# Performance work log

Measured on AMD Instinct MI355X. Metric: run time of the kernel, lower is better.

## Reference

```python
import jax, jax.numpy as jnp
import numpy as np

EPS_LN = 1e-6
EPS_COS = 1e-8  # torch F.cosine_similarity default eps


def setup_inputs() -> dict:
    key = jax.random.key(0)
    ks = jax.random.split(key, 6)
    in_dim, hidden, out_dim, b = 1024, 512, 128, 8192
    x = jax.random.normal(ks[0], (b, in_dim), dtype=jnp.float32)
    # Linear layers: torch default init ~ U(-1/sqrt(fan_in), 1/sqrt(fan_in))
    w1 = jax.random.uniform(ks[1], (in_dim, hidden), jnp.float32, -1, 1) / np.sqrt(in_dim)
    b1 = jax.random.uniform(ks[2], (hidden,), jnp.float32, -1, 1) / np.sqrt(in_dim)
    w2 = jax.random.uniform(ks[3], (hidden, out_dim), jnp.float32, -1, 1) / np.sqrt(hidden)
    b2 = jax.random.uniform(ks[4], (out_dim,), jnp.float32, -1, 1) / np.sqrt(hidden)
    prelu_a = jnp.float32(0.25)  # nn.PReLU default: single shared parameter, init 0.25
    ln_gamma = jnp.ones((hidden,), jnp.float32)
    ln_beta = jnp.zeros((hidden,), jnp.float32)
    return {"x": x, "w1": w1, "b1": b1, "prelu_a": prelu_a,
            "ln_gamma": ln_gamma, "ln_beta": ln_beta, "w2": w2, "b2": b2}


def _layer_norm(h, gamma, beta):
    mu = jnp.mean(h, axis=-1, keepdims=True)
    var = jnp.mean(jnp.square(h - mu), axis=-1, keepdims=True)
    return (h - mu) * jax.lax.rsqrt(var + EPS_LN) * gamma + beta


def reference(x, w1, b1, prelu_a, ln_gamma, ln_beta, w2, b2):
    h = x @ w1 + b1                              # [b, hidden]
    h = jnp.where(h >= 0, h, prelu_a * h)        # PReLU
    h = _layer_norm(h, ln_gamma, ln_beta)        # Dropout is identity in reference
    z = h @ w2 + b2                              # [b, out_dim]
    # get_y_hat: full pairwise cosine similarity as normalize + Gram matmul
    norms = jnp.maximum(jnp.linalg.norm(z, axis=1, keepdims=True), EPS_COS)
    zn = z / norms                               # [b, out_dim]
    y_hat = zn @ zn.T                            # [b, b]
    return z, y_hat
```

## Files before the change

kernel.cpp:

```cpp
#include <hip/hip_runtime.h>
#include <stdint.h>

typedef uint16_t u16;
typedef __bf16 bf16x8 __attribute__((ext_vector_type(8)));
typedef float f32x4 __attribute__((ext_vector_type(4)));

__device__ __forceinline__ u16 f2bf(float f) {
  union { float f; uint32_t u; } v; v.f = f;
  uint32_t u = v.u;
  u += 0x7FFFu + ((u >> 16) & 1u);
  return (u16)(u >> 16);
}
__device__ __forceinline__ float bf2f(u16 h) {
  union { uint32_t u; float f; } v; v.u = ((uint32_t)h) << 16; return v.f;
}

__global__ void transpose_both(const float* __restrict__ w1, u16* __restrict__ w1t,
                               const float* __restrict__ w2, u16* __restrict__ w2t) {
  const float* in; u16* out; int R, C;
  if (blockIdx.z == 0) { in = w1; out = w1t; R = 1024; C = 512; }
  else {
    if (blockIdx.x >= 4 || blockIdx.y >= 16) return;
    in = w2; out = w2t; R = 512; C = 128;
  }
  __shared__ float tile[32][33];
  int bx = blockIdx.x * 32, by = blockIdx.y * 32;
  int tx = threadIdx.x, ty = threadIdx.y;
  for (int i = 0; i < 32; i += 8)
    tile[ty + i][tx] = in[(size_t)(by + ty + i) * C + bx + tx];
  __syncthreads();
  for (int i = 0; i < 32; i += 8)
    out[(size_t)(bx + ty + i) * R + by + tx] = f2bf(tile[tx][ty + i]);
}

#define BKT 64

__launch_bounds__(256)
__global__ void gemm1_kernel(const float* __restrict__ A,
                             const u16* __restrict__ Bt,
                             const float* __restrict__ bias,
                             const float* __restrict__ prelu_a,
                             u16* __restrict__ out) {
  const int N = 512, K = 1024;
  __shared__ u16 As[64][BKT + 8];
  __shared__ u16 Bs[128][BKT + 8];
  const int lane = threadIdx.x & 63, wave = threadIdx.x >> 6;
  const int row0 = blockIdx.x * 64, col0 = blockIdx.y * 128;

  f32x4 zero4 = {0.f, 0.f, 0.f, 0.f};
  f32x4 acc[8];
#pragma unroll
  for (int j = 0; j < 8; ++j) acc[j] = zero4;

  for (int k0 = 0; k0 < K; k0 += BKT) {
#pragma unroll
    for (int s = 0; s < 2; ++s) {
      int c = threadIdx.x + s * 256;
      int r = c >> 3, kc = (c & 7) << 3;
      const float4* p = (const float4*)(A + (size_t)(row0 + r) * K + k0 + kc);
      float4 f0 = p[0], f1 = p[1];
      u16 tmp[8] = {f2bf(f0.x), f2bf(f0.y), f2bf(f0.z), f2bf(f0.w),
                    f2bf(f1.x), f2bf(f1.y), f2bf(f1.z), f2bf(f1.w)};
      *(uint4*)(&As[r][kc]) = *(uint4*)tmp;
    }
#pragma unroll
    for (int s = 0; s < 4; ++s) {
      int c = threadIdx.x + s * 256;
      int r = c >> 3, kc = (c & 7) << 3;
      *(uint4*)(&Bs[r][kc]) = *(const uint4*)(Bt + (size_t)(col0 + r) * K + k0 + kc);
    }
    __syncthreads();
#pragma unroll
    for (int kk = 0; kk < BKT; kk += 32) {
      bf16x8 a, b[8];
      a = *(const bf16x8*)(&As[wave * 16 + (lane & 15)][kk + (lane >> 4) * 8]);
#pragma unroll
      for (int j = 0; j < 8; ++j)
        b[j] = *(const bf16x8*)(&Bs[j * 16 + (lane & 15)][kk + (lane >> 4) * 8]);
#pragma unroll
      for (int j = 0; j < 8; ++j)
        acc[j] = __builtin_amdgcn_mfma_f32_16x16x32_bf16(a, b[j], acc[j], 0, 0, 0);
    }
    __syncthreads();
  }

  float ap = *prelu_a;
#pragma unroll
  for (int r = 0; r < 4; ++r) {
    int row = row0 + wave * 16 + (lane >> 4) * 4 + r;
#pragma unroll
    for (int j = 0; j < 8; ++j) {
      int col = col0 + j * 16 + (lane & 15);
      float v = acc[j][r] + bias[col];
      v = v >= 0.f ? v : ap * v;
      out[(size_t)row * N + col] = f2bf(v);
    }
  }
}

__launch_bounds__(256)
__global__ void ln_kernel(const u16* __restrict__ h, const float* __restrict__ gamma,
                          const float* __restrict__ beta, u16* __restrict__ out) {
  int lane = threadIdx.x & 63, wave = threadIdx.x >> 6;
  int row = blockIdx.x * 4 + wave;
  uint4 raw = *(const uint4*)(h + (size_t)row * 512 + lane * 8);
  u16* up = (u16*)&raw;
  float v[8], s = 0.f, s2 = 0.f;
#pragma unroll
  for (int e = 0; e < 8; ++e) { v[e] = bf2f(up[e]); s += v[e]; s2 += v[e] * v[e]; }
  for (int m = 1; m < 64; m <<= 1) { s += __shfl_xor(s, m); s2 += __shfl_xor(s2, m); }
  float mu = s * (1.f / 512.f);
  float var = s2 * (1.f / 512.f) - mu * mu;
  float rstd = rsqrtf(var + 1e-6f);
  u16 o[8];
#pragma unroll
  for (int e = 0; e < 8; ++e) {
    int c = lane * 8 + e;
    o[e] = f2bf((v[e] - mu) * rstd * gamma[c] + beta[c]);
  }
  *(uint4*)(out + (size_t)row * 512 + lane * 8) = *(uint4*)o;
}

__launch_bounds__(256)
__global__ void gemm2_kernel(const u16* __restrict__ A, const u16* __restrict__ Bt,
                             const float* __restrict__ bias,
                             float* __restrict__ z, u16* __restrict__ zn) {
  const int K = 512;
  __shared__ u16 As[32][BKT + 8];
  __shared__ u16 Bs[128][BKT + 8];
  __shared__ float hsum[32][2];
  const int lane = threadIdx.x & 63, wave = threadIdx.x >> 6;
  const int wr = wave >> 1, wc = wave & 1;
  const int row0 = blockIdx.x * 32;

  f32x4 zero4 = {0.f, 0.f, 0.f, 0.f};
  f32x4 acc[4];
#pragma unroll
  for (int j = 0; j < 4; ++j) acc[j] = zero4;

  for (int k0 = 0; k0 < K; k0 += BKT) {
    {
      int r = threadIdx.x >> 3, kc = (threadIdx.x & 7) << 3;
      *(uint4*)(&As[r][kc]) = *(const uint4*)(A + (size_t)(row0 + r) * K + k0 + kc);
    }
#pragma unroll
    for (int s = 0; s < 4; ++s) {
      int c = threadIdx.x + s * 256;
      int r = c >> 3, kc = (c & 7) << 3;
      *(uint4*)(&Bs[r][kc]) = *(const uint4*)(Bt + (size_t)r * K + k0 + kc);
    }
    __syncthreads();
#pragma unroll
    for (int kk = 0; kk < BKT; kk += 32) {
      bf16x8 a, b[4];
      a = *(const bf16x8*)(&As[wr * 16 + (lane & 15)][kk + (lane >> 4) * 8]);
#pragma unroll
      for (int j = 0; j < 4; ++j)
        b[j] = *(const bf16x8*)(&Bs[wc * 64 + j * 16 + (lane & 15)][kk + (lane >> 4) * 8]);
#pragma unroll
      for (int j = 0; j < 4; ++j)
        acc[j] = __builtin_amdgcn_mfma_f32_16x16x32_bf16(a, b[j], acc[j], 0, 0, 0);
    }
    __syncthreads();
  }

  float vv[4][4];
#pragma unroll
  for (int r = 0; r < 4; ++r) {
    float s = 0.f;
#pragma unroll
    for (int j = 0; j < 4; ++j) {
      int col = wc * 64 + j * 16 + (lane & 15);
      float v = acc[j][r] + bias[col];
      vv[r][j] = v; s += v * v;
    }
    s += __shfl_xor(s, 1); s += __shfl_xor(s, 2);
    s += __shfl_xor(s, 4); s += __shfl_xor(s, 8);
    if ((lane & 15) == 0) {
      int rloc = wr * 16 + (lane >> 4) * 4 + r;
      hsum[rloc][wc] = s;
    }
  }
  __syncthreads();
#pragma unroll
  for (int r = 0; r < 4; ++r) {
    int rloc = wr * 16 + (lane >> 4) * 4 + r;
    float s = hsum[rloc][0] + hsum[rloc][1];
    float inv = 1.f / fmaxf(sqrtf(s), 1e-8f);
    int row = row0 + rloc;
#pragma unroll
    for (int j = 0; j < 4; ++j) {
      int col = wc * 64 + j * 16 + (lane & 15);
      z[(size_t)row * 128 + col] = vv[r][j];
      zn[(size_t)row * 128 + col] = f2bf(vv[r][j] * inv);
    }
  }
}

#define GBM 128
#define GBN 128

__launch_bounds__(256)
__global__ void gram_kernel(const u16* __restrict__ Z, float* __restrict__ y) {
  const int K = 128, Bdim = 8192;
  __shared__ u16 As[GBM][BKT + 8];
  __shared__ u16 Bs[GBN][BKT + 8];
  const int lane = threadIdx.x & 63, wave = threadIdx.x >> 6;
  const int row0 = blockIdx.x * GBM, col0 = blockIdx.y * GBN;

  f32x4 zero4 = {0.f, 0.f, 0.f, 0.f};
  f32x4 acc[2][8];
#pragma unroll
  for (int i = 0; i < 2; ++i)
#pragma unroll
    for (int j = 0; j < 8; ++j) acc[i][j] = zero4;

  for (int k0 = 0; k0 < K; k0 += BKT) {
#pragma unroll
    for (int s = 0; s < 4; ++s) {
      int c = threadIdx.x + s * 256;
      int r = c >> 3, kc = (c & 7) << 3;
      *(uint4*)(&As[r][kc]) = *(const uint4*)(Z + (size_t)(row0 + r) * K + k0 + kc);
      *(uint4*)(&Bs[r][kc]) = *(const uint4*)(Z + (size_t)(col0 + r) * K + k0 + kc);
    }
    __syncthreads();
#pragma unroll
    for (int kk = 0; kk < BKT; kk += 32) {
      bf16x8 a[2], b[8];
#pragma unroll
      for (int i = 0; i < 2; ++i)
        a[i] = *(const bf16x8*)(&As[wave * 32 + i * 16 + (lane & 15)][kk + (lane >> 4) * 8]);
#pragma unroll
      for (int j = 0; j < 8; ++j)
        b[j] = *(const bf16x8*)(&Bs[j * 16 + (lane & 15)][kk + (lane >> 4) * 8]);
#pragma unroll
      for (int i = 0; i < 2; ++i)
#pragma unroll
        for (int j = 0; j < 8; ++j)
          acc[i][j] = __builtin_amdgcn_mfma_f32_16x16x32_bf16(a[i], b[j], acc[i][j], 0, 0, 0);
    }
    __syncthreads();
  }

#pragma unroll
  for (int i = 0; i < 2; ++i)
#pragma unroll
    for (int r = 0; r < 4; ++r) {
      int row = row0 + wave * 32 + i * 16 + (lane >> 4) * 4 + r;
#pragma unroll
      for (int j = 0; j < 8; ++j) {
        int col = col0 + j * 16 + (lane & 15);
        y[(size_t)row * Bdim + col] = acc[i][j][r];
      }
    }
}

extern "C" void kernel_launch(void* const* d_in, const int* in_sizes, int n_in,
                              void* d_out, int out_size, void* d_ws, size_t ws_size,
                              hipStream_t stream) {
  const float* x       = (const float*)d_in[0];
  const float* w1      = (const float*)d_in[1];
  const float* b1      = (const float*)d_in[2];
  const float* prelu_a = (const float*)d_in[3];
  const float* gamma   = (const float*)d_in[4];
  const float* beta    = (const float*)d_in[5];
  const float* w2      = (const float*)d_in[6];
  const float* b2      = (const float*)d_in[7];

  float* z_out = (float*)d_out;
  float* yhat  = z_out + (size_t)8192 * 128;

  char* ws = (char*)d_ws;
  u16* w1t  = (u16*)(ws);
  u16* w2t  = (u16*)(ws + (1u << 20));
  u16* hact = (u16*)(ws + (1u << 20) + (1u << 17));
  u16* hln  = (u16*)(ws + (1u << 20) + (1u << 17) + (8u << 20));
  u16* zn   = (u16*)(ws + (1u << 20) + (1u << 17) + (16u << 20));

  transpose_both<<<dim3(16, 32, 2), dim3(32, 8), 0, stream>>>(w1, w1t, w2, w2t);
  gemm1_kernel<<<dim3(128, 4), 256, 0, stream>>>(x, w1t, b1, prelu_a, hact);
  ln_kernel<<<2048, 256, 0, stream>>>(hact, gamma, beta, hln);
  gemm2_kernel<<<256, 256, 0, stream>>>(hln, w2t, b2, z_out, zn);
  gram_kernel<<<dim3(64, 64), 256, 0, stream>>>(zn, yhat);
}
```

Measured before the change: 362.6 us.

## Fold LayerNorm into gemm2 via algebraic mean/rstd correction

```diff
diff --git a/kernel.cpp b/kernel.cpp
--- a/kernel.cpp
+++ b/kernel.cpp
@@ -16,7 +16,23 @@
 }
 
 __global__ void transpose_both(const float* __restrict__ w1, u16* __restrict__ w1t,
-                               const float* __restrict__ w2, u16* __restrict__ w2t) {
+                               const float* __restrict__ w2, u16* __restrict__ w2t,
+                               const float* __restrict__ gamma,
+                               const float* __restrict__ beta,
+                               float* __restrict__ gw2, float* __restrict__ bw2) {
+  if (blockIdx.z == 2) {
+    if (blockIdx.x || blockIdx.y) return;
+    int tid = threadIdx.y * 32 + threadIdx.x;
+    if (tid < 128) {
+      float g = 0.f, b = 0.f;
+      for (int k = 0; k < 512; ++k) {
+        float w = bf2f(f2bf(w2[(size_t)k * 128 + tid]));
+        g += gamma[k] * w; b += beta[k] * w;
+      }
+      gw2[tid] = g; bw2[tid] = b;
+    }
+    return;
+  }
   const float* in; u16* out; int R, C;
   if (blockIdx.z == 0) { in = w1; out = w1t; R = 1024; C = 512; }
   else {
@@ -99,35 +115,17 @@
 }
 
 __launch_bounds__(256)
-__global__ void ln_kernel(const u16* __restrict__ h, const float* __restrict__ gamma,
-                          const float* __restrict__ beta, u16* __restrict__ out) {
-  int lane = threadIdx.x & 63, wave = threadIdx.x >> 6;
-  int row = blockIdx.x * 4 + wave;
-  uint4 raw = *(const uint4*)(h + (size_t)row * 512 + lane * 8);
-  u16* up = (u16*)&raw;
-  float v[8], s = 0.f, s2 = 0.f;
-#pragma unroll
-  for (int e = 0; e < 8; ++e) { v[e] = bf2f(up[e]); s += v[e]; s2 += v[e] * v[e]; }
-  for (int m = 1; m < 64; m <<= 1) { s += __shfl_xor(s, m); s2 += __shfl_xor(s2, m); }
-  float mu = s * (1.f / 512.f);
-  float var = s2 * (1.f / 512.f) - mu * mu;
-  float rstd = rsqrtf(var + 1e-6f);
-  u16 o[8];
-#pragma unroll
-  for (int e = 0; e < 8; ++e) {
-    int c = lane * 8 + e;
-    o[e] = f2bf((v[e] - mu) * rstd * gamma[c] + beta[c]);
-  }
-  *(uint4*)(out + (size_t)row * 512 + lane * 8) = *(uint4*)o;
-}
-
-__launch_bounds__(256)
 __global__ void gemm2_kernel(const u16* __restrict__ A, const u16* __restrict__ Bt,
-                             const float* __restrict__ bias,
+                             const float* __restrict__ b2,
+                             const float* __restrict__ gamma,
+                             const float* __restrict__ gw2,
+                             const float* __restrict__ bw2,
                              float* __restrict__ z, u16* __restrict__ zn) {
   const int K = 512;
   __shared__ u16 As[32][BKT + 8];
   __shared__ u16 Bs[128][BKT + 8];
+  __shared__ float rs[32][8], rs2[32][8];
+  __shared__ float mu_s[32], rstd_s[32];
   __shared__ float hsum[32][2];
   const int lane = threadIdx.x & 63, wave = threadIdx.x >> 6;
   const int wr = wave >> 1, wc = wave & 1;
@@ -138,10 +136,21 @@
 #pragma unroll
   for (int j = 0; j < 4; ++j) acc[j] = zero4;
 
+  const int ar = threadIdx.x >> 3, akc = (threadIdx.x & 7) << 3;
+  float sp = 0.f, sp2 = 0.f;
+
   for (int k0 = 0; k0 < K; k0 += BKT) {
     {
-      int r = threadIdx.x >> 3, kc = (threadIdx.x & 7) << 3;
-      *(uint4*)(&As[r][kc]) = *(const uint4*)(A + (size_t)(row0 + r) * K + k0 + kc);
+      uint4 raw = *(const uint4*)(A + (size_t)(row0 + ar) * K + k0 + akc);
+      u16* up = (u16*)&raw;
+      u16 tmp[8];
+#pragma unroll
+      for (int e = 0; e < 8; ++e) {
+        float v = bf2f(up[e]);
+        sp += v; sp2 += v * v;
+        tmp[e] = f2bf(v * gamma[k0 + akc + e]);
+      }
+      *(uint4*)(&As[ar][akc]) = *(uint4*)tmp;
     }
 #pragma unroll
     for (int s = 0; s < 4; ++s) {
@@ -164,22 +173,35 @@
     __syncthreads();
   }
 
+  rs[ar][threadIdx.x & 7] = sp;
+  rs2[ar][threadIdx.x & 7] = sp2;
+  __syncthreads();
+  if (threadIdx.x < 32) {
+    float S = 0.f, Q = 0.f;
+#pragma unroll
+    for (int t = 0; t < 8; ++t) { S += rs[threadIdx.x][t]; Q += rs2[threadIdx.x][t]; }
+    float mu = S * (1.f / 512.f);
+    float var = Q * (1.f / 512.f) - mu * mu;
+    mu_s[threadIdx.x] = mu;
+    rstd_s[threadIdx.x] = rsqrtf(var + 1e-6f);
+  }
+  __syncthreads();
+
   float vv[4][4];
 #pragma unroll
   for (int r = 0; r < 4; ++r) {
+    int rloc = wr * 16 + (lane >> 4) * 4 + r;
+    float mu = mu_s[rloc], rstd = rstd_s[rloc];
     float s = 0.f;
 #pragma unroll
     for (int j = 0; j < 4; ++j) {
       int col = wc * 64 + j * 16 + (lane & 15);
-      float v = acc[j][r] + bias[col];
+      float v = rstd * acc[j][r] - mu * rstd * gw2[col] + bw2[col] + b2[col];
       vv[r][j] = v; s += v * v;
     }
     s += __shfl_xor(s, 1); s += __shfl_xor(s, 2);
     s += __shfl_xor(s, 4); s += __shfl_xor(s, 8);
-    if ((lane & 15) == 0) {
-      int rloc = wr * 16 + (lane >> 4) * 4 + r;
-      hsum[rloc][wc] = s;
-    }
+    if ((lane & 15) == 0) hsum[rloc][wc] = s;
   }
   __syncthreads();
 #pragma unroll
@@ -274,12 +296,13 @@
   u16* w1t  = (u16*)(ws);
   u16* w2t  = (u16*)(ws + (1u << 20));
   u16* hact = (u16*)(ws + (1u << 20) + (1u << 17));
-  u16* hln  = (u16*)(ws + (1u << 20) + (1u << 17) + (8u << 20));
-  u16* zn   = (u16*)(ws + (1u << 20) + (1u << 17) + (16u << 20));
-
-  transpose_both<<<dim3(16, 32, 2), dim3(32, 8), 0, stream>>>(w1, w1t, w2, w2t);
+  u16* zn   = (u16*)(ws + (1u << 20) + (1u << 17) + (8u << 20));
+  float* gw2 = (float*)(ws + (1u << 20) + (1u << 17) + (10u << 20));
+  float* bw2 = (float*)(ws + (1u << 20) + (1u << 17) + (10u << 20) + 512);
+
+  transpose_both<<<dim3(16, 32, 3), dim3(32, 8), 0, stream>>>(
+      w1, w1t, w2, w2t, gamma, beta, gw2, bw2);
   gemm1_kernel<<<dim3(128, 4), 256, 0, stream>>>(x, w1t, b1, prelu_a, hact);
-  ln_kernel<<<2048, 256, 0, stream>>>(hact, gamma, beta, hln);
-  gemm2_kernel<<<256, 256, 0, stream>>>(hln, w2t, b2, z_out, zn);
+  gemm2_kernel<<<256, 256, 0, stream>>>(hact, w2t, b2, gamma, gw2, bw2, z_out, zn);
   gram_kernel<<<dim3(64, 64), 256, 0, stream>>>(zn, yhat);
 }
```

Result: slower. 381.8 us (+5.3%).
